# Optimization experiments

Hardware: AMD Instinct MI355X
Metric: run time of the kernel (lower is better)

## Reference

```python
import jax, jax.numpy as jnp
import numpy as np


def _ste(q, x):
    # straight-through estimator: forward = q, gradient = identity w.r.t. x
    return x + jax.lax.stop_gradient(q - x)


def quant_w(w, bit_w=8):
    # symmetric per-tensor weight quantization fused into QConv2d
    qmax = 2.0 ** (bit_w - 1) - 1.0
    scale = jnp.max(jnp.abs(w)) / qmax
    q = jnp.clip(jnp.round(w / scale), -qmax, qmax) * scale
    return _ste(q, w)


def quant_a(x, bit_a=8):
    # unsigned activation quantizer: clamp to [0,1], uniform bit_a levels
    n = 2.0 ** bit_a - 1.0
    xc = jnp.clip(x, 0.0, 1.0)
    q = jnp.round(xc * n) / n
    return _ste(q, xc)


def exp_norm2d(x, gamma, beta, eps=1e-5):
    # instance-style norm: per (N, C) statistics over spatial dims, affine
    mean = jnp.mean(x, axis=(2, 3), keepdims=True)
    var = jnp.var(x, axis=(2, 3), keepdims=True)
    xn = (x - mean) * jax.lax.rsqrt(var + eps)
    return xn * gamma[None, :, None, None] + beta[None, :, None, None]


def qconv(x, w, stride, pad, bit_w=8):
    wq = quant_w(w, bit_w)
    return jax.lax.conv_general_dilated(
        x, wq, window_strides=(stride, stride),
        padding=[(pad, pad), (pad, pad)],
        dimension_numbers=('NCHW', 'OIHW', 'NCHW'))


def setup_inputs() -> dict:
    key = jax.random.key(0)
    ks = jax.random.split(key, 4)
    C_in, C_out, H = 256, 512, 56
    return {
        'x': jax.random.normal(ks[0], (32, C_in, H, H), jnp.float32),
        'w1': jax.random.normal(ks[1], (C_out, C_in, 3, 3), jnp.float32) * 0.05,
        'g1': jnp.ones((C_out,), jnp.float32),
        'b1': jnp.zeros((C_out,), jnp.float32),
        'w2': jax.random.normal(ks[2], (C_out, C_out, 3, 3), jnp.float32) * 0.05,
        'g2': jnp.ones((C_out,), jnp.float32),
        'b2': jnp.zeros((C_out,), jnp.float32),
        'wp': jax.random.normal(ks[3], (C_out, C_in, 1, 1), jnp.float32) * 0.05,
        'gp': jnp.ones((C_out,), jnp.float32),
        'bp': jnp.zeros((C_out,), jnp.float32),
    }


def reference(x, w1, g1, b1, w2, g2, b2, wp, gp, bp):
    # main branch: QConv(s2) -> ExpNorm -> act quant -> QConv(s1) -> ExpNorm
    h = qconv(x, w1, stride=2, pad=1)
    h = exp_norm2d(h, g1, b1)
    h = quant_a(h, bit_a=8)
    h = qconv(h, w2, stride=1, pad=1)
    h = exp_norm2d(h, g2, b2)
    # projection shortcut: QConv 1x1 stride 2 -> ExpNorm
    s = qconv(x, wp, stride=2, pad=0)
    s = exp_norm2d(s, gp, bp)
    return h + s
```

## Files before the change

### kernel.cpp

```cpp
#include <hip/hip_runtime.h>
#include <cstdint>
#include <cstddef>


typedef unsigned short ushort_t;
typedef __attribute__((ext_vector_type(8))) short bf16x8;
typedef __attribute__((ext_vector_type(4))) float f32x4;
typedef __attribute__((ext_vector_type(4))) int i32x4;

#define NB   32
#define C_IN 256
#define HIN  56
#define CO   512
#define OHW  784
#define OWD  28
#define MTOT (NB * OHW)

constexpr size_t OFF_XH   = 0;
constexpr size_t OFF_A1   = OFF_XH  + 51380224;
constexpr size_t OFF_H2   = OFF_A1  + 25690112;
constexpr size_t OFF_S    = OFF_H2  + 51380224;
constexpr size_t OFF_WT1  = OFF_S   + 51380224;
constexpr size_t OFF_WT2  = OFF_WT1 + 2359296;
constexpr size_t OFF_WTP  = OFF_WT2 + 4718592;
constexpr size_t OFF_PSUM = OFF_WTP + 262144;
constexpr size_t OFF_A1N  = OFF_PSUM + 2097152;
constexpr size_t OFF_B1N  = OFF_A1N + 65536;
constexpr size_t OFF_A2N  = OFF_B1N + 65536;
constexpr size_t OFF_B2N  = OFF_A2N + 65536;
constexpr size_t OFF_APN  = OFF_B2N + 65536;
constexpr size_t OFF_BPN  = OFF_APN + 65536;
constexpr size_t OFF_MX   = OFF_BPN + 65536;
constexpr size_t OFF_ZB   = OFF_MX  + 16;
constexpr size_t OFF_CS   = OFF_ZB  + 2048;

__device__ __forceinline__ ushort_t f2bf(float f) {
    unsigned u = __float_as_uint(f);
    u += 0x7FFFu + ((u >> 16) & 1u);
    return (ushort_t)(u >> 16);
}
__device__ __forceinline__ float bf2f(ushort_t u) {
    return __uint_as_float(((unsigned)u) << 16);
}

__device__ __forceinline__ void async_copy16(const void* g, const void* l) {
    auto gp = (const __attribute__((address_space(1))) unsigned int*)(uintptr_t)g;
    auto lp = (__attribute__((address_space(3))) unsigned int*)(unsigned int)(uintptr_t)l;
    __builtin_amdgcn_global_load_lds(gp, lp, 16, 0, 0);
}

__global__ void to_nhwc_k(const float* __restrict__ x, ushort_t* __restrict__ xh) {
    __shared__ float tile[64][33];
    const int wt0 = blockIdx.x * 32;
    const int ct0 = blockIdx.y * 64;
    const int nh  = blockIdx.z;
    const int n = nh / HIN, h = nh - n * HIN;
    {
        const int tx = threadIdx.x & 31;
        const int ty = threadIdx.x >> 5;
        const int w  = wt0 + tx;
#pragma unroll
        for (int j = 0; j < 8; ++j) {
            int cl = ty + j * 8;
            if (w < HIN)
                tile[cl][tx] = x[(((size_t)n * C_IN + ct0 + cl) * HIN + h) * HIN + w];
        }
    }
    __syncthreads();
    {
        const int tc = threadIdx.x & 63;
        const int tw = threadIdx.x >> 6;
#pragma unroll
        for (int j = 0; j < 8; ++j) {
            int wl = tw + j * 4;
            int w  = wt0 + wl;
            if (w < HIN)
                xh[(((size_t)n * HIN + h) * HIN + w) * C_IN + ct0 + tc] =
                    f2bf(tile[tc][wl]);
        }
    }
}

__global__ void absmax3_k(const float* __restrict__ w1, int n1,
                          const float* __restrict__ w2, int n2,
                          const float* __restrict__ wp, int np,
                          unsigned* out) {
    const float* w; int nelem;
    if (blockIdx.y == 0)      { w = w1; nelem = n1; }
    else if (blockIdx.y == 1) { w = w2; nelem = n2; }
    else                      { w = wp; nelem = np; }
    int stride = gridDim.x * blockDim.x;
    float m = 0.f;
    for (int i = blockIdx.x * blockDim.x + threadIdx.x; i < nelem; i += stride)
        m = fmaxf(m, fabsf(w[i]));
#pragma unroll
    for (int off = 32; off > 0; off >>= 1)
        m = fmaxf(m, __shfl_down(m, off));
    if ((threadIdx.x & 63) == 0) atomicMax(out + blockIdx.y, __float_as_uint(m));
}

template <int CO_, int CI_, int KHW_>
__global__ void quantw_k(const float* __restrict__ w, const unsigned* __restrict__ mx,
                         ushort_t* __restrict__ wt) {
    const int total = KHW_ * CO_ * CI_;
    int idx = blockIdx.x * 256 + threadIdx.x;
    if (idx >= total) return;
    float scale = __uint_as_float(*mx) * (1.0f / 127.0f);
    float inv   = scale > 0.f ? 1.0f / scale : 0.f;
    int khw = idx / (CO_ * CI_);
    int r   = idx - khw * (CO_ * CI_);
    int co  = r / CI_;
    int ci  = r - co * CI_;
    float v  = w[((size_t)co * CI_ + ci) * KHW_ + khw];
    float qv = rintf(v * inv);
    qv = fminf(127.f, fmaxf(-127.f, qv));
    wt[idx] = f2bf(qv * scale);
}

__global__ void quantw_i8_k(const float* __restrict__ w, const unsigned* __restrict__ mx,
                            signed char* __restrict__ wt, float* __restrict__ cs) {
    int idx = blockIdx.x * 256 + threadIdx.x;
    float scale = __uint_as_float(*mx) * (1.0f / 127.0f);
    float inv   = scale > 0.f ? 1.0f / scale : 0.f;
    int khw = idx / (CO * CO);
    int r   = idx - khw * (CO * CO);
    int co  = r / CO;
    int ci  = r - co * CO;
    float v  = w[((size_t)co * CO + ci) * 9 + khw];
    float qv = rintf(v * inv);
    qv = fminf(127.f, fmaxf(-127.f, qv));
    int iq = (int)qv;
    wt[idx] = (signed char)iq;
    int s = iq;
#pragma unroll
    for (int off = 32; off > 0; off >>= 1)
        s += __shfl_down(s, off);
    if ((threadIdx.x & 63) == 0) atomicAdd(&cs[khw * CO + co], (float)s);
}

template <int CIN, int KH, int KW, int STRIDE, int PAD, int IH, int IW>
__launch_bounds__(512, 2)
__global__ void conv8p_k(const ushort_t* __restrict__ xin,
                         const ushort_t* __restrict__ wt,
                         ushort_t* __restrict__ out,
                         const ushort_t* __restrict__ zbuf,
                         float* __restrict__ psum, float* __restrict__ pss) {
    constexpr int BK  = 64;
    constexpr int CKT = CIN / BK;
    constexpr int KT  = KH * KW * CKT;

    __shared__ alignas(16) short As[2 * 256 * BK];
    __shared__ alignas(16) short Bs[2 * 256 * BK];

    const int tid  = threadIdx.x;
    const int lane = tid & 63;
    const int wv   = tid >> 6;
    const int wm   = wv >> 2;
    const int wn   = wv & 3;
    const int lrow = lane & 15;
    const int lq   = lane >> 4;
    const int sw   = lrow & 7;

    const int bid = blockIdx.x;
    const int xcd = bid & 7;
    const int j   = bid >> 3;
    const int wg  = (xcd < 4 ? xcd * 25 : 100 + (xcd - 4) * 24) + j;
    const int m0  = (wg >> 1) * 256;
    const int co0 = (wg & 1) * 256;

    const int arow = tid >> 3;
    const int ach  = tid & 7;
    long abase[4]; unsigned amask[4]; int bco[4];
#pragma unroll
    for (int c = 0; c < 4; ++c) {
        int row = c * 64 + arow;
        int m   = m0 + row;
        int n   = m / OHW;
        int sp  = m - n * OHW;
        int oh  = sp / OWD, ow = sp - oh * OWD;
        int ihb = oh * STRIDE - PAD, iwb = ow * STRIDE - PAD;
        int swz = (ach ^ (row & 7)) * 8;
        abase[c] = ((long)n * (IH * IW) + (long)ihb * IW + iwb) * CIN + swz;
        unsigned mk = 0;
#pragma unroll
        for (int kh = 0; kh < KH; ++kh)
#pragma unroll
            for (int kw = 0; kw < KW; ++kw) {
                int ih = ihb + kh, iw = iwb + kw;
                if ((unsigned)ih < (unsigned)IH && (unsigned)iw < (unsigned)IW)
                    mk |= 1u << (kh * KW + kw);
            }
        amask[c] = mk;
        bco[c]   = (co0 + row) * CIN + swz;
    }

    auto stageA = [&](int c, int nb, long aoff, int khw) {
        const ushort_t* src = ((amask[c] >> khw) & 1)
            ? xin + (abase[c] + aoff) : zbuf;
        async_copy16(src, (const void*)&As[nb * 16384 + c * 4096 + wv * 512]);
    };
    auto stageB = [&](int c, int nb, int boff) {
        async_copy16(wt + (boff + bco[c]),
                     (const void*)&Bs[nb * 16384 + c * 4096 + wv * 512]);
    };

    f32x4 acc[8][4];
#pragma unroll
    for (int a = 0; a < 8; ++a)
#pragma unroll
        for (int b = 0; b < 4; ++b) acc[a][b] = {0.f, 0.f, 0.f, 0.f};

    stageB(0, 0, 0); stageB(1, 0, 0); stageB(2, 0, 0); stageB(3, 0, 0);
    stageA(0, 0, 0, 0); stageA(1, 0, 0, 0); stageA(2, 0, 0, 0); stageA(3, 0, 0, 0);
    asm volatile("s_waitcnt vmcnt(0)" ::: "memory");
    __builtin_amdgcn_s_barrier();

    int  khw_n = 0, kw_n = 0, ck_n = 1;
    long aoff_n = BK;
    int  boff_n = BK;

    int cur = 0;
    for (int t = 0; t < KT; ++t) {
        const bool hn = (t + 1 < KT);
        const int  nb = cur ^ 1;
        const short* Acur = &As[cur * 16384];
        const short* Bcur = &Bs[cur * 16384];

        if (hn) {
            stageB(0, nb, boff_n); stageB(1, nb, boff_n);
            stageB(2, nb, boff_n); stageB(3, nb, boff_n);
            stageA(0, nb, aoff_n, khw_n); stageA(1, nb, aoff_n, khw_n);
            stageA(2, nb, aoff_n, khw_n); stageA(3, nb, aoff_n, khw_n);
        }
        __builtin_amdgcn_sched_barrier(0);

        bf16x8 af[4][2], bfr[2][2][2];

#pragma unroll
        for (int mi = 0; mi < 4; ++mi) {
            const int row = wm * 128 + mi * 16 + lrow;
#pragma unroll
            for (int ks = 0; ks < 2; ++ks) {
                const int ch = ((ks * 4 + lq) ^ sw) * 8;
                af[mi][ks] = *(const bf16x8*)&Acur[row * BK + ch];
            }
        }
#pragma unroll
        for (int qn = 0; qn < 2; ++qn)
#pragma unroll
            for (int ni = 0; ni < 2; ++ni) {
                const int row = wn * 64 + qn * 32 + ni * 16 + lrow;
#pragma unroll
                for (int ks = 0; ks < 2; ++ks) {
                    const int ch = ((ks * 4 + lq) ^ sw) * 8;
                    bfr[qn][ni][ks] = *(const bf16x8*)&Bcur[row * BK + ch];
                }
            }
#pragma unroll
        for (int mi = 0; mi < 4; ++mi)
#pragma unroll
            for (int qn = 0; qn < 2; ++qn)
#pragma unroll
                for (int ni = 0; ni < 2; ++ni)
#pragma unroll
                    for (int ks = 0; ks < 2; ++ks)
                        acc[mi][qn * 2 + ni] =
                            __builtin_amdgcn_mfma_f32_16x16x32_bf16(
                                af[mi][ks], bfr[qn][ni][ks],
                                acc[mi][qn * 2 + ni], 0, 0, 0);

#pragma unroll
        for (int mi = 0; mi < 4; ++mi) {
            const int row = wm * 128 + 64 + mi * 16 + lrow;
#pragma unroll
            for (int ks = 0; ks < 2; ++ks) {
                const int ch = ((ks * 4 + lq) ^ sw) * 8;
                af[mi][ks] = *(const bf16x8*)&Acur[row * BK + ch];
            }
        }
#pragma unroll
        for (int mi = 0; mi < 4; ++mi)
#pragma unroll
            for (int qn = 0; qn < 2; ++qn)
#pragma unroll
                for (int ni = 0; ni < 2; ++ni)
#pragma unroll
                    for (int ks = 0; ks < 2; ++ks)
                        acc[4 + mi][qn * 2 + ni] =
                            __builtin_amdgcn_mfma_f32_16x16x32_bf16(
                                af[mi][ks], bfr[qn][ni][ks],
                                acc[4 + mi][qn * 2 + ni], 0, 0, 0);

        asm volatile("s_waitcnt vmcnt(0)" ::: "memory");
        __builtin_amdgcn_sched_barrier(0);
        __builtin_amdgcn_s_barrier();

        if (hn) {
            ck_n++;
            if (ck_n == CKT) {
                ck_n = 0; khw_n++; kw_n++;
                if (kw_n == KW) { kw_n = 0; aoff_n += (long)(IW - KW) * CIN + BK; }
                else            { aoff_n += BK; }
                boff_n += (CO - 1) * CIN + BK;
            } else {
                aoff_n += BK; boff_n += BK;
            }
        }
        cur ^= 1;
    }

    const int mb = m0 + wm * 128 + lq * 4;
    const int cb = co0 + wn * 64 + lrow;
#pragma unroll
    for (int mi = 0; mi < 8; ++mi)
#pragma unroll
        for (int ni = 0; ni < 4; ++ni)
#pragma unroll
            for (int r = 0; r < 4; ++r)
                out[(size_t)(mb + mi * 16 + r) * CO + (cb + ni * 16)] =
                    f2bf(acc[mi][ni][r]);

    const int n0 = m0 / OHW;
    const int mS = (n0 + 1) * OHW;
    float sv[2][4], qv[2][4];
#pragma unroll
    for (int g = 0; g < 2; ++g)
#pragma unroll
        for (int ni = 0; ni < 4; ++ni) { sv[g][ni] = 0.f; qv[g][ni] = 0.f; }
#pragma unroll
    for (int mi = 0; mi < 8; ++mi)
#pragma unroll
        for (int ni = 0; ni < 4; ++ni)
#pragma unroll
            for (int r = 0; r < 4; ++r) {
                float v = acc[mi][ni][r];
                int m = mb + mi * 16 + r;
                int g = (m >= mS) ? 1 : 0;
                sv[g][ni] += v; qv[g][ni] += v * v;
            }
#pragma unroll
    for (int d = 16; d <= 32; d <<= 1)
#pragma unroll
        for (int g = 0; g < 2; ++g)
#pragma unroll
            for (int ni = 0; ni < 4; ++ni) {
                sv[g][ni] += __shfl_xor(sv[g][ni], d);
                qv[g][ni] += __shfl_xor(qv[g][ni], d);
            }
    if (lq == 0) {
        const bool split = (mS < m0 + 256);
#pragma unroll
        for (int ni = 0; ni < 4; ++ni) {
            atomicAdd(&psum[n0 * CO + cb + ni * 16], sv[0][ni]);
            atomicAdd(&pss [n0 * CO + cb + ni * 16], qv[0][ni]);
            if (split) {
                atomicAdd(&psum[(n0 + 1) * CO + cb + ni * 16], sv[1][ni]);
                atomicAdd(&pss [(n0 + 1) * CO + cb + ni * 16], qv[1][ni]);
            }
        }
    }
}

__launch_bounds__(1024, 4)
__global__ void conv_i8_k(const signed char* __restrict__ xin,
                          const signed char* __restrict__ wt,
                          const float* __restrict__ colsum,
                          const unsigned* __restrict__ mxp,
                          ushort_t* __restrict__ out,
                          const signed char* __restrict__ zbuf,
                          float* __restrict__ psum, float* __restrict__ pss) {
    constexpr int CIN = 512, BK = 64, CKT = 8, KT = 72;
    constexpr int IH = 28, IW = 28;

    __shared__ alignas(16) signed char As[2 * 256 * BK];
    __shared__ alignas(16) signed char Bs[2 * 256 * BK];

    const int tid  = threadIdx.x;
    const int lane = tid & 63;
    const int wv   = tid >> 6;
    const int wm   = wv >> 2;
    const int wn   = wv & 3;
    const int lrow = lane & 15;
    const int lq   = lane >> 4;

    const int bid = blockIdx.x;
    const int xcd = bid & 7;
    const int j   = bid >> 3;
    const int wg  = (xcd < 4 ? xcd * 25 : 100 + (xcd - 4) * 24) + j;
    const int m0  = (wg >> 1) * 256;
    const int co0 = (wg & 1) * 256;

    const int arow = tid >> 2;
    const int ach  = tid & 3;
    int abase; unsigned amask; int bco;
    {
        int m   = m0 + arow;
        int n   = m / OHW;
        int sp  = m - n * OHW;
        int oh  = sp / OWD, ow = sp - oh * OWD;
        int ihb = oh - 1, iwb = ow - 1;
        int swz = (ach ^ ((arow >> 1) & 3)) * 16;
        abase = (n * (IH * IW) + ihb * IW + iwb) * CIN + swz;
        unsigned mk = 0;
#pragma unroll
        for (int kh = 0; kh < 3; ++kh)
#pragma unroll
            for (int kw = 0; kw < 3; ++kw) {
                int ih = ihb + kh, iw = iwb + kw;
                if ((unsigned)ih < (unsigned)IH && (unsigned)iw < (unsigned)IW)
                    mk |= 1u << (kh * 3 + kw);
            }
        amask = mk;
        bco = (co0 + arow) * CIN + swz;
    }

    auto stageA = [&](int nb, int aoff, int khw) {
        const signed char* src = ((amask >> khw) & 1)
            ? xin + (abase + aoff) : zbuf;
        async_copy16(src, (const void*)&As[nb * 16384 + wv * 1024]);
    };
    auto stageB = [&](int nb, int boff) {
        async_copy16(wt + (boff + bco), (const void*)&Bs[nb * 16384 + wv * 1024]);
    };

    i32x4 acc[4][4];
#pragma unroll
    for (int a = 0; a < 4; ++a)
#pragma unroll
        for (int b = 0; b < 4; ++b) acc[a][b] = {0, 0, 0, 0};

    stageB(0, 0);
    stageA(0, 0, 0);
    asm volatile("s_waitcnt vmcnt(0)" ::: "memory");
    __builtin_amdgcn_s_barrier();

    int khw_n = 0, kw_n = 0, ck_n = 1;
    int aoff_n = BK;
    int boff_n = BK;

    int cur = 0;
    for (int t = 0; t < KT; ++t) {
        const bool hn = (t + 1 < KT);
        const int  nb = cur ^ 1;
        const signed char* Acur = &As[cur * 16384];
        const signed char* Bcur = &Bs[cur * 16384];

        if (hn) { stageB(nb, boff_n); stageA(nb, aoff_n, khw_n); }
        __builtin_amdgcn_sched_barrier(0);

        i32x4 af[4], bfr[4];
#pragma unroll
        for (int mi = 0; mi < 4; ++mi) {
            const int row = wm * 64 + mi * 16 + lrow;
            af[mi] = *(const i32x4*)&Acur[row * BK + ((lq ^ ((row >> 1) & 3)) * 16)];
        }
#pragma unroll
        for (int ni = 0; ni < 4; ++ni) {
            const int row = wn * 64 + ni * 16 + lrow;
            bfr[ni] = *(const i32x4*)&Bcur[row * BK + ((lq ^ ((row >> 1) & 3)) * 16)];
        }
#pragma unroll
        for (int mi = 0; mi < 4; ++mi)
#pragma unroll
            for (int ni = 0; ni < 4; ++ni)
                acc[mi][ni] = __builtin_amdgcn_mfma_i32_16x16x64_i8(
                    af[mi], bfr[ni], acc[mi][ni], 0, 0, 0);

        asm volatile("s_waitcnt vmcnt(0)" ::: "memory");
        __builtin_amdgcn_sched_barrier(0);
        __builtin_amdgcn_s_barrier();

        if (hn) {
            ck_n++;
            if (ck_n == CKT) {
                ck_n = 0; khw_n++; kw_n++;
                if (kw_n == 3) { kw_n = 0; aoff_n += (IW - 3) * CIN + BK; }
                else           { aoff_n += BK; }
                boff_n += (CO - 1) * CIN + BK;
            } else {
                aoff_n += BK; boff_n += BK;
            }
        }
        cur ^= 1;
    }

    const int mb = m0 + wm * 64 + lq * 4;
    const int cb = co0 + wn * 64 + lrow;
    const float scale = __uint_as_float(*mxp) * (1.0f / 127.0f);
    const float sc    = scale * (1.0f / 255.0f);
    const float c128  = 128.0f * sc;

    float Sall[4], Sr0[4], Sr2[4], Sc0[4], Sc2[4], K0[4], K2[4], K6[4], K8[4];
#pragma unroll
    for (int ni = 0; ni < 4; ++ni) {
        float cs[9];
#pragma unroll
        for (int k = 0; k < 9; ++k) cs[k] = colsum[k * CO + cb + ni * 16];
        Sall[ni] = cs[0]+cs[1]+cs[2]+cs[3]+cs[4]+cs[5]+cs[6]+cs[7]+cs[8];
        Sr0[ni] = cs[0]+cs[1]+cs[2];  Sr2[ni] = cs[6]+cs[7]+cs[8];
        Sc0[ni] = cs[0]+cs[3]+cs[6];  Sc2[ni] = cs[2]+cs[5]+cs[8];
        K0[ni] = cs[0]; K2[ni] = cs[2]; K6[ni] = cs[6]; K8[ni] = cs[8];
    }

    const int n0 = m0 / OHW;
    const int mS = (n0 + 1) * OHW;
    float sv[2][4], qvv[2][4];
#pragma unroll
    for (int g = 0; g < 2; ++g)
#pragma unroll
        for (int ni = 0; ni < 4; ++ni) { sv[g][ni] = 0.f; qvv[g][ni] = 0.f; }

#pragma unroll
    for (int mi = 0; mi < 4; ++mi)
#pragma unroll
        for (int r = 0; r < 4; ++r) {
            const int m  = mb + mi * 16 + r;
            const int n  = m / OHW;
            const int sp = m - n * OHW;
            const int oh = sp / OWD, ow = sp - oh * OWD;
            const int g  = (m >= mS) ? 1 : 0;
#pragma unroll
            for (int ni = 0; ni < 4; ++ni) {
                float T = Sall[ni];
                if (oh == 0)       T -= Sr0[ni];
                if (oh == OWD - 1) T -= Sr2[ni];
                if (ow == 0)       T -= Sc0[ni];
                if (ow == OWD - 1) T -= Sc2[ni];
                if (oh == 0 && ow == 0)             T += K0[ni];
                if (oh == 0 && ow == OWD - 1)       T += K2[ni];
                if (oh == OWD - 1 && ow == 0)       T += K6[ni];
                if (oh == OWD - 1 && ow == OWD - 1) T += K8[ni];
                float val = sc * (float)acc[mi][ni][r] + c128 * T;
                out[(size_t)m * CO + (cb + ni * 16)] = f2bf(val);
                sv[g][ni] += val; qvv[g][ni] += val * val;
            }
        }
#pragma unroll
    for (int d = 16; d <= 32; d <<= 1)
#pragma unroll
        for (int g = 0; g < 2; ++g)
#pragma unroll
            for (int ni = 0; ni < 4; ++ni) {
                sv[g][ni]  += __shfl_xor(sv[g][ni], d);
                qvv[g][ni] += __shfl_xor(qvv[g][ni], d);
            }
    if (lq == 0) {
        const bool split = (mS < m0 + 256);
#pragma unroll
        for (int ni = 0; ni < 4; ++ni) {
            atomicAdd(&psum[n0 * CO + cb + ni * 16], sv[0][ni]);
            atomicAdd(&pss [n0 * CO + cb + ni * 16], qvv[0][ni]);
            if (split) {
                atomicAdd(&psum[(n0 + 1) * CO + cb + ni * 16], sv[1][ni]);
                atomicAdd(&pss [(n0 + 1) * CO + cb + ni * 16], qvv[1][ni]);
            }
        }
    }
}

__global__ void statsf3_k(const float* __restrict__ ps0, const float* __restrict__ qs0,
                          const float* __restrict__ g0, const float* __restrict__ bb0,
                          float* __restrict__ ao0, float* __restrict__ bo0,
                          const float* __restrict__ ps1, const float* __restrict__ qs1,
                          const float* __restrict__ g1, const float* __restrict__ bb1,
                          float* __restrict__ ao1, float* __restrict__ bo1,
                          const float* __restrict__ ps2, const float* __restrict__ qs2,
                          const float* __restrict__ g2, const float* __restrict__ bb2,
                          float* __restrict__ ao2, float* __restrict__ bo2) {
    const float *ps, *qs, *g, *bb; float *ao, *bo;
    if (blockIdx.y == 0)      { ps = ps0; qs = qs0; g = g0; bb = bb0; ao = ao0; bo = bo0; }
    else if (blockIdx.y == 1) { ps = ps1; qs = qs1; g = g1; bb = bb1; ao = ao1; bo = bo1; }
    else                      { ps = ps2; qs = qs2; g = g2; bb = bb2; ao = ao2; bo = bo2; }
    int idx = blockIdx.x * 256 + threadIdx.x;
    int c = idx & 511;
    float s  = ps[idx];
    float ss = qs[idx];
    float mean = s * (1.0f / 784.0f);
    float var  = ss * (1.0f / 784.0f) - mean * mean;
    float rstd = rsqrtf(var + 1e-5f);
    float a = rstd * g[c];
    ao[idx] = a;
    bo[idx] = bb[c] - mean * a;
}

__global__ void norm_quant_i8_k(const ushort_t* __restrict__ h, const float* __restrict__ a_,
                                const float* __restrict__ b_, signed char* __restrict__ o) {
    int idx = blockIdx.x * 256 + threadIdx.x;
    int row = idx >> 6;
    int c0  = (idx & 63) * 8;
    int n   = row / OHW;
    bf16x8 v = ((const bf16x8*)h)[idx];
    const float* ap = a_ + n * CO + c0;
    const float* bp = b_ + n * CO + c0;
    unsigned lo = 0, hi = 0;
#pragma unroll
    for (int k = 0; k < 8; ++k) {
        float f = bf2f((ushort_t)v[k]) * ap[k] + bp[k];
        float kq = rintf(fminf(fmaxf(f, 0.f), 1.f) * 255.f);
        int s8 = (int)kq - 128;
        unsigned b = (unsigned)(s8 & 0xFF);
        if (k < 4) lo |= b << (8 * k);
        else       hi |= b << (8 * (k - 4));
    }
    ((uint2*)o)[idx] = make_uint2(lo, hi);
}

__global__ void final_k(const ushort_t* __restrict__ h2, const ushort_t* __restrict__ s,
                        const float* __restrict__ a2, const float* __restrict__ b2,
                        const float* __restrict__ ap_, const float* __restrict__ bp_,
                        float* __restrict__ out) {
    __shared__ float tile[64][33];
    const int sp0 = blockIdx.x * 32;
    const int c0  = blockIdx.y * 64;
    const int n   = blockIdx.z;
    const int tx  = threadIdx.x & 31;
    const int ty  = threadIdx.x >> 5;
#pragma unroll
    for (int j = 0; j < 4; ++j) {
        int spl = ty + j * 8;
        int sp  = sp0 + spl;
        if (sp < OHW) {
            int c = c0 + tx * 2;
            size_t ix = ((size_t)n * OHW + sp) * CO + c;
            int ci = n * CO + c;
            ushort2 vh = *(const ushort2*)&h2[ix];
            ushort2 vs = *(const ushort2*)&s[ix];
            tile[tx * 2][spl] =
                bf2f(vh.x) * a2[ci] + b2[ci] + bf2f(vs.x) * ap_[ci] + bp_[ci];
            tile[tx * 2 + 1][spl] =
                bf2f(vh.y) * a2[ci + 1] + b2[ci + 1] + bf2f(vs.y) * ap_[ci + 1] + bp_[ci + 1];
        }
    }
    __syncthreads();
    const int sp = sp0 + tx;
#pragma unroll
    for (int j = 0; j < 8; ++j) {
        int cl = ty + j * 8;
        if (sp < OHW)
            out[((size_t)n * CO + c0 + cl) * OHW + sp] = tile[cl][tx];
    }
}

extern "C" void kernel_launch(void* const* d_in, const int* in_sizes, int n_in,
                              void* d_out, int out_size, void* d_ws, size_t ws_size,
                              hipStream_t stream) {
    const float* x  = (const float*)d_in[0];
    const float* w1 = (const float*)d_in[1];
    const float* g1 = (const float*)d_in[2];
    const float* b1 = (const float*)d_in[3];
    const float* w2 = (const float*)d_in[4];
    const float* g2 = (const float*)d_in[5];
    const float* b2 = (const float*)d_in[6];
    const float* wp = (const float*)d_in[7];
    const float* gp = (const float*)d_in[8];
    const float* bp = (const float*)d_in[9];
    float* out = (float*)d_out;
    char* ws = (char*)d_ws;

    ushort_t*    xh    = (ushort_t*)(ws + OFF_XH);
    signed char* a1    = (signed char*)(ws + OFF_A1);
    ushort_t*    h2    = (ushort_t*)(ws + OFF_H2);
    ushort_t*    sbuf  = (ushort_t*)(ws + OFF_S);
    ushort_t*    wt1   = (ushort_t*)(ws + OFF_WT1);
    signed char* wt2i  = (signed char*)(ws + OFF_WT2);
    ushort_t*    wtp   = (ushort_t*)(ws + OFF_WTP);
    float*    psum1 = (float*)(ws + OFF_PSUM);
    float*    pss1  = (float*)(ws + OFF_PSUM + 65536);
    float*    psum2 = (float*)(ws + OFF_PSUM + 131072);
    float*    pss2  = (float*)(ws + OFF_PSUM + 196608);
    float*    psump = (float*)(ws + OFF_PSUM + 262144);
    float*    pssp  = (float*)(ws + OFF_PSUM + 327680);
    float*    a1n  = (float*)(ws + OFF_A1N);
    float*    b1n  = (float*)(ws + OFF_B1N);
    float*    a2n  = (float*)(ws + OFF_A2N);
    float*    b2n  = (float*)(ws + OFF_B2N);
    float*    apn  = (float*)(ws + OFF_APN);
    float*    bpn  = (float*)(ws + OFF_BPN);
    unsigned* mx   = (unsigned*)(ws + OFF_MX);
    ushort_t* zb   = (ushort_t*)(ws + OFF_ZB);
    float*    cs   = (float*)(ws + OFF_CS);
    ushort_t* h1   = (ushort_t*)out;

    hipMemsetAsync(ws + OFF_MX, 0, 16 + 2048 + 18432, stream);
    hipMemsetAsync(ws + OFF_PSUM, 0, 393216, stream);

    to_nhwc_k<<<dim3(2, 4, NB * HIN), 256, 0, stream>>>(x, xh);
    absmax3_k<<<dim3(512, 3), 256, 0, stream>>>(w1, CO * C_IN * 9,
                                                w2, CO * CO * 9,
                                                wp, C_IN * CO, mx);
    quantw_k<CO, C_IN, 9><<<dim3(4608), 256, 0, stream>>>(w1, mx + 0, wt1);
    quantw_i8_k<<<dim3(9216), 256, 0, stream>>>(w2, mx + 1, wt2i, cs);
    quantw_k<CO, C_IN, 1><<<dim3(512), 256, 0, stream>>>(wp, mx + 2, wtp);

    conv8p_k<C_IN, 3, 3, 2, 1, HIN, HIN>
        <<<dim3(196), 512, 0, stream>>>(xh, wt1, h1, (const ushort_t*)zb, psum1, pss1);
    statsf3_k<<<dim3(64, 1), 256, 0, stream>>>(psum1, pss1, g1, b1, a1n, b1n,
                                               psum1, pss1, g1, b1, a1n, b1n,
                                               psum1, pss1, g1, b1, a1n, b1n);
    norm_quant_i8_k<<<dim3(MTOT * CO / 8 / 256), 256, 0, stream>>>(h1, a1n, b1n, a1);

    conv_i8_k<<<dim3(196), 1024, 0, stream>>>(a1, wt2i, cs, mx + 1, h2,
                                              (const signed char*)zb, psum2, pss2);
    conv8p_k<C_IN, 1, 1, 2, 0, HIN, HIN>
        <<<dim3(196), 512, 0, stream>>>(xh, wtp, sbuf, (const ushort_t*)zb, psump, pssp);

    statsf3_k<<<dim3(64, 2), 256, 0, stream>>>(psum2, pss2, g2, b2, a2n, b2n,
                                               psump, pssp, gp, bp, apn, bpn,
                                               psum2, pss2, g2, b2, a2n, b2n);

    final_k<<<dim3(25, 8, NB), 256, 0, stream>>>(h2, sbuf, a2n, b2n, apn, bpn, out);
}
```

Baseline: 320.5 us.

## Deepen int8 conv pipeline to four buffers and fuse weight-quant launches

The int8 3x3 conv now uses four LDS stages and processes two K-steps per barrier, prefetching two steps ahead to reduce sync overhead and hide load latency. The three weight quantization kernels are merged into one launch, and the zero-initialised buffers are made contiguous so one memset replaces two. The larger LDS footprint limits residency to one block per CU.

```diff
diff --git a/kernel.cpp b/kernel.cpp
--- a/kernel.cpp
+++ b/kernel.cpp
@@ -23,8 +23,7 @@
 constexpr size_t OFF_WT1  = OFF_S   + 51380224;
 constexpr size_t OFF_WT2  = OFF_WT1 + 2359296;
 constexpr size_t OFF_WTP  = OFF_WT2 + 4718592;
-constexpr size_t OFF_PSUM = OFF_WTP + 262144;
-constexpr size_t OFF_A1N  = OFF_PSUM + 2097152;
+constexpr size_t OFF_A1N  = OFF_WTP + 262144;
 constexpr size_t OFF_B1N  = OFF_A1N + 65536;
 constexpr size_t OFF_A2N  = OFF_B1N + 65536;
 constexpr size_t OFF_B2N  = OFF_A2N + 65536;
@@ -33,6 +32,8 @@
 constexpr size_t OFF_MX   = OFF_BPN + 65536;
 constexpr size_t OFF_ZB   = OFF_MX  + 16;
 constexpr size_t OFF_CS   = OFF_ZB  + 2048;
+constexpr size_t OFF_PSUM = OFF_CS  + 18432;
+constexpr size_t ZERO_LEN = 16 + 2048 + 18432 + 393216;
 
 __device__ __forceinline__ ushort_t f2bf(float f) {
     unsigned u = __float_as_uint(f);
@@ -99,43 +100,56 @@
     if ((threadIdx.x & 63) == 0) atomicMax(out + blockIdx.y, __float_as_uint(m));
 }
 
-template <int CO_, int CI_, int KHW_>
-__global__ void quantw_k(const float* __restrict__ w, const unsigned* __restrict__ mx,
-                         ushort_t* __restrict__ wt) {
-    const int total = KHW_ * CO_ * CI_;
-    int idx = blockIdx.x * 256 + threadIdx.x;
-    if (idx >= total) return;
-    float scale = __uint_as_float(*mx) * (1.0f / 127.0f);
-    float inv   = scale > 0.f ? 1.0f / scale : 0.f;
-    int khw = idx / (CO_ * CI_);
-    int r   = idx - khw * (CO_ * CI_);
-    int co  = r / CI_;
-    int ci  = r - co * CI_;
-    float v  = w[((size_t)co * CI_ + ci) * KHW_ + khw];
-    float qv = rintf(v * inv);
-    qv = fminf(127.f, fmaxf(-127.f, qv));
-    wt[idx] = f2bf(qv * scale);
-}
-
-__global__ void quantw_i8_k(const float* __restrict__ w, const unsigned* __restrict__ mx,
-                            signed char* __restrict__ wt, float* __restrict__ cs) {
-    int idx = blockIdx.x * 256 + threadIdx.x;
-    float scale = __uint_as_float(*mx) * (1.0f / 127.0f);
-    float inv   = scale > 0.f ? 1.0f / scale : 0.f;
-    int khw = idx / (CO * CO);
-    int r   = idx - khw * (CO * CO);
-    int co  = r / CO;
-    int ci  = r - co * CO;
-    float v  = w[((size_t)co * CO + ci) * 9 + khw];
-    float qv = rintf(v * inv);
-    qv = fminf(127.f, fmaxf(-127.f, qv));
-    int iq = (int)qv;
-    wt[idx] = (signed char)iq;
-    int s = iq;
-#pragma unroll
-    for (int off = 32; off > 0; off >>= 1)
-        s += __shfl_down(s, off);
-    if ((threadIdx.x & 63) == 0) atomicAdd(&cs[khw * CO + co], (float)s);
+__global__ void quantw_all_k(const float* __restrict__ w1,
+                             const float* __restrict__ w2,
+                             const float* __restrict__ wp,
+                             const unsigned* __restrict__ mx,
+                             ushort_t* __restrict__ wt1,
+                             signed char* __restrict__ wt2,
+                             ushort_t* __restrict__ wtp,
+                             float* __restrict__ cs) {
+    const int b = blockIdx.x;
+    if (b < 4608) {
+        int idx = b * 256 + threadIdx.x;
+        float scale = __uint_as_float(mx[0]) * (1.0f / 127.0f);
+        float inv   = scale > 0.f ? 1.0f / scale : 0.f;
+        int khw = idx / (CO * C_IN);
+        int r   = idx - khw * (CO * C_IN);
+        int co  = r / C_IN;
+        int ci  = r - co * C_IN;
+        float v  = w1[((size_t)co * C_IN + ci) * 9 + khw];
+        float qv = rintf(v * inv);
+        qv = fminf(127.f, fmaxf(-127.f, qv));
+        wt1[idx] = f2bf(qv * scale);
+    } else if (b < 13824) {
+        int idx = (b - 4608) * 256 + threadIdx.x;
+        float scale = __uint_as_float(mx[1]) * (1.0f / 127.0f);
+        float inv   = scale > 0.f ? 1.0f / scale : 0.f;
+        int khw = idx / (CO * CO);
+        int r   = idx - khw * (CO * CO);
+        int co  = r / CO;
+        int ci  = r - co * CO;
+        float v  = w2[((size_t)co * CO + ci) * 9 + khw];
+        float qv = rintf(v * inv);
+        qv = fminf(127.f, fmaxf(-127.f, qv));
+        int iq = (int)qv;
+        wt2[idx] = (signed char)iq;
+        int s = iq;
+#pragma unroll
+        for (int off = 32; off > 0; off >>= 1)
+            s += __shfl_down(s, off);
+        if ((threadIdx.x & 63) == 0) atomicAdd(&cs[khw * CO + co], (float)s);
+    } else {
+        int idx = (b - 13824) * 256 + threadIdx.x;
+        float scale = __uint_as_float(mx[2]) * (1.0f / 127.0f);
+        float inv   = scale > 0.f ? 1.0f / scale : 0.f;
+        int co  = idx / C_IN;
+        int ci  = idx - co * C_IN;
+        float v  = wp[(size_t)co * C_IN + ci];
+        float qv = rintf(v * inv);
+        qv = fminf(127.f, fmaxf(-127.f, qv));
+        wtp[idx] = f2bf(qv * scale);
+    }
 }
 
 template <int CIN, int KH, int KW, int STRIDE, int PAD, int IH, int IW>
@@ -371,9 +385,10 @@
                           float* __restrict__ psum, float* __restrict__ pss) {
     constexpr int CIN = 512, BK = 64, CKT = 8, KT = 72;
     constexpr int IH = 28, IW = 28;
-
-    __shared__ alignas(16) signed char As[2 * 256 * BK];
-    __shared__ alignas(16) signed char Bs[2 * 256 * BK];
+    constexpr int NPER = KT / 2;
+
+    __shared__ alignas(16) signed char As[4 * 256 * BK];
+    __shared__ alignas(16) signed char Bs[4 * 256 * BK];
 
     const int tid  = threadIdx.x;
     const int lane = tid & 63;
@@ -414,13 +429,13 @@
         bco = (co0 + arow) * CIN + swz;
     }
 
-    auto stageA = [&](int nb, int aoff, int khw) {
+    auto stageA = [&](int buf, int aoff, int khw) {
         const signed char* src = ((amask >> khw) & 1)
             ? xin + (abase + aoff) : zbuf;
-        async_copy16(src, (const void*)&As[nb * 16384 + wv * 1024]);
+        async_copy16(src, (const void*)&As[buf * 16384 + wv * 1024]);
     };
-    auto stageB = [&](int nb, int boff) {
-        async_copy16(wt + (boff + bco), (const void*)&Bs[nb * 16384 + wv * 1024]);
+    auto stageB = [&](int buf, int boff) {
+        async_copy16(wt + (boff + bco), (const void*)&Bs[buf * 16384 + wv * 1024]);
     };
 
     i32x4 acc[4][4];
@@ -429,59 +444,63 @@
 #pragma unroll
         for (int b = 0; b < 4; ++b) acc[a][b] = {0, 0, 0, 0};
 
-    stageB(0, 0);
-    stageA(0, 0, 0);
+    stageB(0, 0);  stageA(0, 0, 0);
+    stageB(1, BK); stageA(1, BK, 0);
     asm volatile("s_waitcnt vmcnt(0)" ::: "memory");
     __builtin_amdgcn_s_barrier();
 
-    int khw_n = 0, kw_n = 0, ck_n = 1;
-    int aoff_n = BK;
-    int boff_n = BK;
-
-    int cur = 0;
-    for (int t = 0; t < KT; ++t) {
-        const bool hn = (t + 1 < KT);
-        const int  nb = cur ^ 1;
-        const signed char* Acur = &As[cur * 16384];
-        const signed char* Bcur = &Bs[cur * 16384];
-
-        if (hn) { stageB(nb, boff_n); stageA(nb, aoff_n, khw_n); }
+    int khw_n = 0, kw_n = 0, ck_n = 2;
+    int aoff_n = 2 * BK;
+    int boff_n = 2 * BK;
+
+#pragma unroll 1
+    for (int p = 0; p < NPER; ++p) {
+        const int t0 = 2 * p;
+        if (p + 1 < NPER) {
+#pragma unroll
+            for (int u = 0; u < 2; ++u) {
+                const int buf = (t0 + 2 + u) & 3;
+                stageB(buf, boff_n);
+                stageA(buf, aoff_n, khw_n);
+                ck_n++;
+                if (ck_n == CKT) {
+                    ck_n = 0; khw_n++; kw_n++;
+                    if (kw_n == 3) { kw_n = 0; aoff_n += (IW - 3) * CIN + BK; }
+                    else           { aoff_n += BK; }
+                    boff_n += (CO - 1) * CIN + BK;
+                } else {
+                    aoff_n += BK; boff_n += BK;
+                }
+            }
+        }
         __builtin_amdgcn_sched_barrier(0);
 
-        i32x4 af[4], bfr[4];
-#pragma unroll
-        for (int mi = 0; mi < 4; ++mi) {
-            const int row = wm * 64 + mi * 16 + lrow;
-            af[mi] = *(const i32x4*)&Acur[row * BK + ((lq ^ ((row >> 1) & 3)) * 16)];
-        }
-#pragma unroll
-        for (int ni = 0; ni < 4; ++ni) {
-            const int row = wn * 64 + ni * 16 + lrow;
-            bfr[ni] = *(const i32x4*)&Bcur[row * BK + ((lq ^ ((row >> 1) & 3)) * 16)];
-        }
-#pragma unroll
-        for (int mi = 0; mi < 4; ++mi)
-#pragma unroll
-            for (int ni = 0; ni < 4; ++ni)
-                acc[mi][ni] = __builtin_amdgcn_mfma_i32_16x16x64_i8(
-                    af[mi], bfr[ni], acc[mi][ni], 0, 0, 0);
+#pragma unroll
+        for (int sub = 0; sub < 2; ++sub) {
+            const signed char* Acur = &As[((t0 + sub) & 3) * 16384];
+            const signed char* Bcur = &Bs[((t0 + sub) & 3) * 16384];
+            i32x4 af[4], bfr[4];
+#pragma unroll
+            for (int mi = 0; mi < 4; ++mi) {
+                const int row = wm * 64 + mi * 16 + lrow;
+                af[mi] = *(const i32x4*)&Acur[row * BK + ((lq ^ ((row >> 1) & 3)) * 16)];
+            }
+#pragma unroll
+            for (int ni = 0; ni < 4; ++ni) {
+                const int row = wn * 64 + ni * 16 + lrow;
+                bfr[ni] = *(const i32x4*)&Bcur[row * BK + ((lq ^ ((row >> 1) & 3)) * 16)];
+            }
+#pragma unroll
+            for (int mi = 0; mi < 4; ++mi)
+#pragma unroll
+                for (int ni = 0; ni < 4; ++ni)
+                    acc[mi][ni] = __builtin_amdgcn_mfma_i32_16x16x64_i8(
+                        af[mi], bfr[ni], acc[mi][ni], 0, 0, 0);
+        }
 
         asm volatile("s_waitcnt vmcnt(0)" ::: "memory");
         __builtin_amdgcn_sched_barrier(0);
         __builtin_amdgcn_s_barrier();
-
-        if (hn) {
-            ck_n++;
-            if (ck_n == CKT) {
-                ck_n = 0; khw_n++; kw_n++;
-                if (kw_n == 3) { kw_n = 0; aoff_n += (IW - 3) * CIN + BK; }
-                else           { aoff_n += BK; }
-                boff_n += (CO - 1) * CIN + BK;
-            } else {
-                aoff_n += BK; boff_n += BK;
-            }
-        }
-        cur ^= 1;
     }
 
     const int mb = m0 + wm * 64 + lq * 4;
@@ -664,12 +683,6 @@
     ushort_t*    wt1   = (ushort_t*)(ws + OFF_WT1);
     signed char* wt2i  = (signed char*)(ws + OFF_WT2);
     ushort_t*    wtp   = (ushort_t*)(ws + OFF_WTP);
-    float*    psum1 = (float*)(ws + OFF_PSUM);
-    float*    pss1  = (float*)(ws + OFF_PSUM + 65536);
-    float*    psum2 = (float*)(ws + OFF_PSUM + 131072);
-    float*    pss2  = (float*)(ws + OFF_PSUM + 196608);
-    float*    psump = (float*)(ws + OFF_PSUM + 262144);
-    float*    pssp  = (float*)(ws + OFF_PSUM + 327680);
     float*    a1n  = (float*)(ws + OFF_A1N);
     float*    b1n  = (float*)(ws + OFF_B1N);
     float*    a2n  = (float*)(ws + OFF_A2N);
@@ -679,18 +692,22 @@
     unsigned* mx   = (unsigned*)(ws + OFF_MX);
     ushort_t* zb   = (ushort_t*)(ws + OFF_ZB);
     float*    cs   = (float*)(ws + OFF_CS);
+    float*    psum1 = (float*)(ws + OFF_PSUM);
+    float*    pss1  = (float*)(ws + OFF_PSUM + 65536);
+    float*    psum2 = (float*)(ws + OFF_PSUM + 131072);
+    float*    pss2  = (float*)(ws + OFF_PSUM + 196608);
+    float*    psump = (float*)(ws + OFF_PSUM + 262144);
+    float*    pssp  = (float*)(ws + OFF_PSUM + 327680);
     ushort_t* h1   = (ushort_t*)out;
 
-    hipMemsetAsync(ws + OFF_MX, 0, 16 + 2048 + 18432, stream);
-    hipMemsetAsync(ws + OFF_PSUM, 0, 393216, stream);
+    hipMemsetAsync(ws + OFF_MX, 0, ZERO_LEN, stream);
 
     to_nhwc_k<<<dim3(2, 4, NB * HIN), 256, 0, stream>>>(x, xh);
     absmax3_k<<<dim3(512, 3), 256, 0, stream>>>(w1, CO * C_IN * 9,
                                                 w2, CO * CO * 9,
                                                 wp, C_IN * CO, mx);
-    quantw_k<CO, C_IN, 9><<<dim3(4608), 256, 0, stream>>>(w1, mx + 0, wt1);
-    quantw_i8_k<<<dim3(9216), 256, 0, stream>>>(w2, mx + 1, wt2i, cs);
-    quantw_k<CO, C_IN, 1><<<dim3(512), 256, 0, stream>>>(wp, mx + 2, wtp);
+    quantw_all_k<<<dim3(14336), 256, 0, stream>>>(w1, w2, wp, mx,
+                                                  wt1, wt2i, wtp, cs);
 
     conv8p_k<C_IN, 3, 3, 2, 1, HIN, HIN>
         <<<dim3(196), 512, 0, stream>>>(xh, wt1, h1, (const ushort_t*)zb, psum1, pss1);
```

Measured after the change: 310.4 us. 1.03x faster.
